# Kernel optimization log

Hardware: AMD Instinct MI355X
Metric: run time of the kernel (lower is better)

## Reference

```python
import jax, jax.numpy as jnp
import numpy as np

TAU = 1.0
NUM_CLASSES = 14
EDGE_W = 500.0
BODY_W = 200.0
LOSS_W = 1.0


def _cross_reduce(x, op, pad_val):
    """Apply op over the 3D 6-neighborhood cross (scipy default structure).
    x: bool [B, C, D, H, W]."""
    p = jnp.pad(x, ((0, 0), (0, 0), (1, 1), (1, 1), (1, 1)), constant_values=pad_val)
    r = p[:, :, 1:-1, 1:-1, 1:-1]
    r = op(r, p[:, :, :-2, 1:-1, 1:-1]); r = op(r, p[:, :, 2:, 1:-1, 1:-1])
    r = op(r, p[:, :, 1:-1, :-2, 1:-1]); r = op(r, p[:, :, 1:-1, 2:, 1:-1])
    r = op(r, p[:, :, 1:-1, 1:-1, :-2]); r = op(r, p[:, :, 1:-1, 1:-1, 2:])
    return r


def _edge_body_masks(gt_labels):
    # gt_labels: int [B, 1, D, H, W] -> bool masks [B, NUM_CLASSES, D, H, W]
    gt = gt_labels[:, 0]  # [B, D, H, W]
    onehot = gt[:, None] == jnp.arange(NUM_CLASSES, dtype=gt.dtype)[None, :, None, None, None]
    # binary_dilation ^ binary_erosion, both with border_value=0 (scipy default)
    dil = _cross_reduce(onehot, jnp.logical_or, False)
    ero = _cross_reduce(onehot, jnp.logical_and, False)
    edges = jnp.logical_xor(dil, ero)
    bodies = jnp.logical_and(jnp.logical_not(edges), onehot)
    # class 0 (background) masks are forced to zero in the original loop
    edges = edges.at[:, 0].set(False)
    bodies = bodies.at[:, 0].set(False)
    return edges, bodies


def _cwd(preds_S, preds_T):
    # ChannelWiseDivergence: per-(batch,channel) softmax over flattened spatial dims
    B, C = preds_S.shape[0], preds_S.shape[1]
    s = preds_S.reshape(B * C, -1) / TAU
    t = preds_T.reshape(B * C, -1) / TAU
    p_t = jax.nn.softmax(t, axis=-1)
    loss = jnp.sum(p_t * (jax.nn.log_softmax(t, axis=-1) - jax.nn.log_softmax(s, axis=-1)))
    return loss * (TAU ** 2) / (B * C)


def setup_inputs() -> dict:
    key = jax.random.key(0)
    k1, k2, k3 = jax.random.split(key, 3)
    B, C, D, H, W = 2, NUM_CLASSES, 96, 96, 96
    preds_S = jax.random.normal(k1, (B, C, D, H, W), dtype=jnp.float32)
    preds_T = jax.random.normal(k2, (B, C, D, H, W), dtype=jnp.float32)
    gt_labels = jax.random.randint(k3, (B, 1, D, H, W), 0, NUM_CLASSES, dtype=jnp.int64)
    return {"preds_S": preds_S, "preds_T": preds_T, "gt_labels": gt_labels}


def reference(preds_S, preds_T, gt_labels):
    B = preds_S.shape[0]
    edges, bodies = _edge_body_masks(gt_labels)
    me = edges.astype(preds_S.dtype)
    mb = bodies.astype(preds_S.dtype)
    loss_edges = _cwd(preds_S * me, preds_T * me) * LOSS_W * EDGE_W / B
    loss_bodies = _cwd(preds_S * mb, preds_T * mb) * LOSS_W * BODY_W / B
    return loss_edges, loss_bodies
```

## Files before the change

kernel.cpp:

```cpp
#include <hip/hip_runtime.h>
#include <math.h>

#define NCLS 14
#define DIMX 96
#define DIMXY (DIMX * DIMX)
#define NVOX (DIMX * DIMX * DIMX)
#define BATCH 2
#define ROWS (BATCH * NCLS)
#define TPB 256
#define BPR 54
#define VPT 16
#define BLK_VOX (TPB * 4 * VPT)
#define PSTRIDE 8

__global__ __launch_bounds__(256) void mask_kernel(const int* __restrict__ gt,
                                                   unsigned* __restrict__ masks) {
    int idx4 = blockIdx.x * 256 + threadIdx.x;
    if (idx4 >= BATCH * NVOX / 4) return;
    int v4 = idx4 * 4;
    int b = v4 / NVOX;
    int v = v4 - b * NVOX;
    int w = v % DIMX;
    int h = (v / DIMX) % DIMX;
    int d = v / DIMXY;
    const int* __restrict__ g = gt + (size_t)b * NVOX;

    int gc[4];
    { int4 t4 = *(const int4*)&g[v]; gc[0] = t4.x; gc[1] = t4.y; gc[2] = t4.z; gc[3] = t4.w; }
    bool hasU = h > 0, hasD = h < DIMX - 1, hasF = d > 0, hasB = d < DIMX - 1;
    bool hasL0 = w > 0;
    bool hasR3 = (w + 3) < DIMX - 1;
    int up[4], dn[4], fr[4], bk[4];
    if (hasU) { int4 t4 = *(const int4*)&g[v - DIMX];  up[0]=t4.x; up[1]=t4.y; up[2]=t4.z; up[3]=t4.w; }
    if (hasD) { int4 t4 = *(const int4*)&g[v + DIMX];  dn[0]=t4.x; dn[1]=t4.y; dn[2]=t4.z; dn[3]=t4.w; }
    if (hasF) { int4 t4 = *(const int4*)&g[v - DIMXY]; fr[0]=t4.x; fr[1]=t4.y; fr[2]=t4.z; fr[3]=t4.w; }
    if (hasB) { int4 t4 = *(const int4*)&g[v + DIMXY]; bk[0]=t4.x; bk[1]=t4.y; bk[2]=t4.z; bk[3]=t4.w; }
    int lf0 = hasL0 ? g[v - 1] : 0;
    int rt3 = hasR3 ? g[v + 4] : 0;

    unsigned res[4];
    #pragma unroll
    for (int j = 0; j < 4; ++j) {
        int c0 = gc[j];
        unsigned dil = 1u << c0;
        bool all = hasU && hasD && hasF && hasB;
        int  lf = (j == 0) ? lf0 : gc[j - 1]; bool hl = (j > 0) || hasL0;
        int  rt = (j == 3) ? rt3 : gc[j + 1]; bool hr = (j < 3) || hasR3;
        all = all && hl && hr;
        if (hl)   { dil |= 1u << lf;    all = all && (lf == c0); }
        if (hr)   { dil |= 1u << rt;    all = all && (rt == c0); }
        if (hasU) { dil |= 1u << up[j]; all = all && (up[j] == c0); }
        if (hasD) { dil |= 1u << dn[j]; all = all && (dn[j] == c0); }
        if (hasF) { dil |= 1u << fr[j]; all = all && (fr[j] == c0); }
        if (hasB) { dil |= 1u << bk[j]; all = all && (bk[j] == c0); }
        unsigned edge = dil & ~1u;
        if (all) edge &= ~(1u << c0);
        unsigned bodyc = (all && c0 != 0) ? (unsigned)c0 : 15u;
        res[j] = edge | (bodyc << 16);
    }
    *(uint4*)&masks[(size_t)v4] = make_uint4(res[0], res[1], res[2], res[3]);
}

__global__ __launch_bounds__(TPB) void cwd_kernel(const float* __restrict__ Sp,
                                                  const float* __restrict__ Tp,
                                                  const unsigned* __restrict__ masks,
                                                  float* __restrict__ partials) {
    int row = blockIdx.x / BPR;
    int blk = blockIdx.x - row * BPR;
    int b = row / NCLS;
    unsigned c = (unsigned)(row - b * NCLS);
    const float* __restrict__ s_ptr = Sp + (size_t)row * NVOX;
    const float* __restrict__ t_ptr = Tp + (size_t)row * NVOX;
    const unsigned* __restrict__ m_ptr = masks + (size_t)b * NVOX;
    int base = blk * BLK_VOX + (int)threadIdx.x * 4;

    float ez[4] = {0.f, 0.f, 0.f, 0.f};
    float es[4] = {0.f, 0.f, 0.f, 0.f};
    float eq[4] = {0.f, 0.f, 0.f, 0.f};
    float bz = 0.f, bs1 = 0.f, bzs = 0.f, bcnt = 0.f;

    #pragma unroll 4
    for (int k = 0; k < VPT; ++k) {
        int v = base + k * (TPB * 4);
        uint4  wm4 = *(const uint4*)&m_ptr[v];
        float4 t4  = *(const float4*)&t_ptr[v];
        float4 s4  = *(const float4*)&s_ptr[v];
        unsigned wms[4] = {wm4.x, wm4.y, wm4.z, wm4.w};
        float    ts[4]  = {t4.x, t4.y, t4.z, t4.w};
        float    ss[4]  = {s4.x, s4.y, s4.z, s4.w};
        #pragma unroll
        for (int j = 0; j < 4; ++j) {
            unsigned wm = wms[j];
            float me = (float)((wm >> c) & 1u);
            float tv = ts[j] * me;
            float sv = ss[j] * me;
            float et = __expf(tv);
            ez[j] += et;
            es[j] += et * (tv - sv);
            eq[j] += __expf(sv);
            if (((wm >> 16) & 0xFu) == c) {
                float bt = __expf(ts[j]);
                bz  += bt;
                bs1 += bt * (ts[j] - ss[j]);
                bzs += __expf(ss[j]);
                bcnt += 1.f;
            }
        }
    }
    float r0 = (ez[0] + ez[1]) + (ez[2] + ez[3]);
    float r1 = (es[0] + es[1]) + (es[2] + es[3]);
    float r2 = (eq[0] + eq[1]) + (eq[2] + eq[3]);
    float r3 = bz, r4 = bs1, r5 = bzs, r6 = bcnt;

    #pragma unroll
    for (int off = 32; off > 0; off >>= 1) {
        r0 += __shfl_down(r0, off);
        r1 += __shfl_down(r1, off);
        r2 += __shfl_down(r2, off);
        r3 += __shfl_down(r3, off);
        r4 += __shfl_down(r4, off);
        r5 += __shfl_down(r5, off);
        r6 += __shfl_down(r6, off);
    }
    __shared__ float red[4][PSTRIDE];
    int wid = (int)threadIdx.x >> 6;
    int lane = (int)threadIdx.x & 63;
    if (lane == 0) {
        red[wid][0] = r0; red[wid][1] = r1; red[wid][2] = r2; red[wid][3] = r3;
        red[wid][4] = r4; red[wid][5] = r5; red[wid][6] = r6;
    }
    __syncthreads();
    if (threadIdx.x < PSTRIDE) {
        int i = (int)threadIdx.x;
        float sum = (i < 7) ? (red[0][i] + red[1][i] + red[2][i] + red[3][i]) : 0.f;
        partials[(size_t)blockIdx.x * PSTRIDE + i] = sum;
    }
}

__global__ __launch_bounds__(64) void final_kernel(const float* __restrict__ partials,
                                                   float* __restrict__ out) {
    __shared__ double se[64], sb[64];
    int r = threadIdx.x;
    double le = 0.0, lb = 0.0;
    if (r < ROWS) {
        double zt = 0.0, s1 = 0.0, zs = 0.0;
        double vbz = 0.0, vbs1 = 0.0, vbzs = 0.0, vbc = 0.0;
        for (int k = 0; k < BPR; ++k) {
            const float* p = partials + (size_t)(r * BPR + k) * PSTRIDE;
            zt  += p[0]; s1  += p[1]; zs  += p[2];
            vbz += p[3]; vbs1 += p[4]; vbzs += p[5]; vbc += p[6];
        }
        le = s1 / zt - log(zt) + log(zs);
        double rem = (double)NVOX - vbc;
        double bzt = vbz + rem, bzs2 = vbzs + rem;
        lb = vbs1 / bzt - log(bzt) + log(bzs2);
    }
    se[r] = le;
    sb[r] = lb;
    __syncthreads();
    if (r == 0) {
        double a = 0.0, c = 0.0;
        for (int i = 0; i < ROWS; ++i) { a += se[i]; c += sb[i]; }
        out[0] = (float)(a * (500.0 / 56.0));
        out[1] = (float)(c * (200.0 / 56.0));
    }
}

extern "C" void kernel_launch(void* const* d_in, const int* in_sizes, int n_in,
                              void* d_out, int out_size, void* d_ws, size_t ws_size,
                              hipStream_t stream) {
    const float* Sp = (const float*)d_in[0];
    const float* Tp = (const float*)d_in[1];
    const int* gt = (const int*)d_in[2];
    float* out = (float*)d_out;

    unsigned* masks = (unsigned*)d_ws;
    float* partials = (float*)((char*)d_ws + (size_t)BATCH * NVOX * sizeof(unsigned));

    hipLaunchKernelGGL(mask_kernel, dim3(BATCH * NVOX / 4 / 256), dim3(256), 0, stream,
                       gt, masks);
    hipLaunchKernelGGL(cwd_kernel, dim3(ROWS * BPR), dim3(TPB), 0, stream,
                       Sp, Tp, masks, partials);
    hipLaunchKernelGGL(final_kernel, dim3(1), dim3(64), 0, stream, partials, out);
}
```

Measured before the change: 52.30 us.

## Process all classes per voxel chunk and accumulate sparse body terms atomically

Each block of the CWD kernel now covers one voxel chunk for all 14 classes of a batch, instead of one class row. The packed mask word is then loaded once per voxel rather than once per class, which removes most of the repeated mask traffic. Body-loss terms are gathered only for the voxel's body class and added to per-row accumulators with global atomics. This relies on body voxels being rare, and adds register pressure from 42 per-thread accumulators plus a wider final reduction.

```diff
diff --git a/kernel.cpp b/kernel.cpp
--- a/kernel.cpp
+++ b/kernel.cpp
@@ -8,13 +8,14 @@
 #define BATCH 2
 #define ROWS (BATCH * NCLS)
 #define TPB 256
-#define BPR 54
-#define VPT 16
-#define BLK_VOX (TPB * 4 * VPT)
-#define PSTRIDE 8
+#define VPT 2
+#define CPB (TPB * 4 * VPT)
+#define NBLK (NVOX / CPB)
 
 __global__ __launch_bounds__(256) void mask_kernel(const int* __restrict__ gt,
-                                                   unsigned* __restrict__ masks) {
+                                                   unsigned* __restrict__ masks,
+                                                   float* __restrict__ body_acc) {
+    if (blockIdx.x == 0 && threadIdx.x < ROWS * 4) body_acc[threadIdx.x] = 0.f;
     int idx4 = blockIdx.x * 256 + threadIdx.x;
     if (idx4 >= BATCH * NVOX / 4) return;
     int v4 = idx4 * 4;
@@ -64,105 +65,122 @@
 __global__ __launch_bounds__(TPB) void cwd_kernel(const float* __restrict__ Sp,
                                                   const float* __restrict__ Tp,
                                                   const unsigned* __restrict__ masks,
-                                                  float* __restrict__ partials) {
-    int row = blockIdx.x / BPR;
-    int blk = blockIdx.x - row * BPR;
-    int b = row / NCLS;
-    unsigned c = (unsigned)(row - b * NCLS);
-    const float* __restrict__ s_ptr = Sp + (size_t)row * NVOX;
-    const float* __restrict__ t_ptr = Tp + (size_t)row * NVOX;
-    const unsigned* __restrict__ m_ptr = masks + (size_t)b * NVOX;
-    int base = blk * BLK_VOX + (int)threadIdx.x * 4;
-
-    float ez[4] = {0.f, 0.f, 0.f, 0.f};
-    float es[4] = {0.f, 0.f, 0.f, 0.f};
-    float eq[4] = {0.f, 0.f, 0.f, 0.f};
-    float bz = 0.f, bs1 = 0.f, bzs = 0.f, bcnt = 0.f;
-
-    #pragma unroll 4
+                                                  float* __restrict__ partials,
+                                                  float* __restrict__ body_acc) {
+    int blk = blockIdx.x;
+    int b = blk / NBLK;
+    int chunk = blk - b * NBLK;
+    const unsigned* __restrict__ mp = masks + (size_t)b * NVOX;
+    const float* __restrict__ tb = Tp + (size_t)b * NCLS * NVOX;
+    const float* __restrict__ sb = Sp + (size_t)b * NCLS * NVOX;
+    int base = chunk * CPB + (int)threadIdx.x * 4;
+
+    float zt[NCLS], s1[NCLS], zs[NCLS];
+    #pragma unroll
+    for (int c = 0; c < NCLS; ++c) { zt[c] = 0.f; s1[c] = 0.f; zs[c] = 0.f; }
+
+    #pragma unroll
     for (int k = 0; k < VPT; ++k) {
         int v = base + k * (TPB * 4);
-        uint4  wm4 = *(const uint4*)&m_ptr[v];
-        float4 t4  = *(const float4*)&t_ptr[v];
-        float4 s4  = *(const float4*)&s_ptr[v];
-        unsigned wms[4] = {wm4.x, wm4.y, wm4.z, wm4.w};
-        float    ts[4]  = {t4.x, t4.y, t4.z, t4.w};
-        float    ss[4]  = {s4.x, s4.y, s4.z, s4.w};
+        uint4 wm4 = *(const uint4*)&mp[v];
+        unsigned wm[4] = {wm4.x, wm4.y, wm4.z, wm4.w};
+        #pragma unroll
+        for (int c = 0; c < NCLS; ++c) {
+            float4 t4 = *(const float4*)&tb[(size_t)c * NVOX + v];
+            float4 s4 = *(const float4*)&sb[(size_t)c * NVOX + v];
+            float tt[4] = {t4.x, t4.y, t4.z, t4.w};
+            float ss[4] = {s4.x, s4.y, s4.z, s4.w};
+            #pragma unroll
+            for (int j = 0; j < 4; ++j) {
+                float me = (float)((wm[j] >> c) & 1u);
+                float tv = tt[j] * me;
+                float sv = ss[j] * me;
+                float et = __expf(tv);
+                zt[c] += et;
+                s1[c] += et * (tv - sv);
+                zs[c] += __expf(sv);
+            }
+        }
         #pragma unroll
         for (int j = 0; j < 4; ++j) {
-            unsigned wm = wms[j];
-            float me = (float)((wm >> c) & 1u);
-            float tv = ts[j] * me;
-            float sv = ss[j] * me;
-            float et = __expf(tv);
-            ez[j] += et;
-            es[j] += et * (tv - sv);
-            eq[j] += __expf(sv);
-            if (((wm >> 16) & 0xFu) == c) {
-                float bt = __expf(ts[j]);
-                bz  += bt;
-                bs1 += bt * (ts[j] - ss[j]);
-                bzs += __expf(ss[j]);
-                bcnt += 1.f;
+            unsigned bc = wm[j] >> 16;
+            if (bc != 15u) {
+                size_t off = (size_t)bc * NVOX + (size_t)(v + j);
+                float t = tb[off], s = sb[off];
+                float* acc = body_acc + ((size_t)b * NCLS + bc) * 4;
+                atomicAdd(acc + 0, __expf(t));
+                atomicAdd(acc + 1, __expf(t) * (t - s));
+                atomicAdd(acc + 2, __expf(s));
+                atomicAdd(acc + 3, 1.f);
             }
         }
     }
-    float r0 = (ez[0] + ez[1]) + (ez[2] + ez[3]);
-    float r1 = (es[0] + es[1]) + (es[2] + es[3]);
-    float r2 = (eq[0] + eq[1]) + (eq[2] + eq[3]);
-    float r3 = bz, r4 = bs1, r5 = bzs, r6 = bcnt;
 
     #pragma unroll
     for (int off = 32; off > 0; off >>= 1) {
-        r0 += __shfl_down(r0, off);
-        r1 += __shfl_down(r1, off);
-        r2 += __shfl_down(r2, off);
-        r3 += __shfl_down(r3, off);
-        r4 += __shfl_down(r4, off);
-        r5 += __shfl_down(r5, off);
-        r6 += __shfl_down(r6, off);
-    }
-    __shared__ float red[4][PSTRIDE];
+        #pragma unroll
+        for (int c = 0; c < NCLS; ++c) {
+            zt[c] += __shfl_down(zt[c], off);
+            s1[c] += __shfl_down(s1[c], off);
+            zs[c] += __shfl_down(zs[c], off);
+        }
+    }
+    __shared__ float red[4][NCLS * 3];
     int wid = (int)threadIdx.x >> 6;
     int lane = (int)threadIdx.x & 63;
     if (lane == 0) {
-        red[wid][0] = r0; red[wid][1] = r1; red[wid][2] = r2; red[wid][3] = r3;
-        red[wid][4] = r4; red[wid][5] = r5; red[wid][6] = r6;
+        #pragma unroll
+        for (int c = 0; c < NCLS; ++c) {
+            red[wid][c * 3 + 0] = zt[c];
+            red[wid][c * 3 + 1] = s1[c];
+            red[wid][c * 3 + 2] = zs[c];
+        }
     }
     __syncthreads();
-    if (threadIdx.x < PSTRIDE) {
+    if (threadIdx.x < NCLS * 3) {
         int i = (int)threadIdx.x;
-        float sum = (i < 7) ? (red[0][i] + red[1][i] + red[2][i] + red[3][i]) : 0.f;
-        partials[(size_t)blockIdx.x * PSTRIDE + i] = sum;
-    }
-}
-
-__global__ __launch_bounds__(64) void final_kernel(const float* __restrict__ partials,
-                                                   float* __restrict__ out) {
-    __shared__ double se[64], sb[64];
-    int r = threadIdx.x;
-    double le = 0.0, lb = 0.0;
-    if (r < ROWS) {
+        float s = (red[0][i] + red[1][i]) + (red[2][i] + red[3][i]);
+        partials[(size_t)blk * (NCLS * 3) + i] = s;
+    }
+}
+
+__global__ __launch_bounds__(1024) void final_kernel(const float* __restrict__ partials,
+                                                     const float* __restrict__ body_acc,
+                                                     float* __restrict__ out) {
+    int tid = (int)threadIdx.x;
+    int row = tid >> 5;
+    int sub = tid & 31;
+    __shared__ double les[ROWS], lbs[ROWS];
+    if (row < ROWS) {
+        int b = row / NCLS, c = row - b * NCLS;
         double zt = 0.0, s1 = 0.0, zs = 0.0;
-        double vbz = 0.0, vbs1 = 0.0, vbzs = 0.0, vbc = 0.0;
-        for (int k = 0; k < BPR; ++k) {
-            const float* p = partials + (size_t)(r * BPR + k) * PSTRIDE;
-            zt  += p[0]; s1  += p[1]; zs  += p[2];
-            vbz += p[3]; vbs1 += p[4]; vbzs += p[5]; vbc += p[6];
-        }
-        le = s1 / zt - log(zt) + log(zs);
-        double rem = (double)NVOX - vbc;
-        double bzt = vbz + rem, bzs2 = vbzs + rem;
-        lb = vbs1 / bzt - log(bzt) + log(bzs2);
-    }
-    se[r] = le;
-    sb[r] = lb;
+        for (int k = sub; k < NBLK; k += 32) {
+            const float* p = partials + (size_t)(b * NBLK + k) * (NCLS * 3) + c * 3;
+            zt += (double)p[0]; s1 += (double)p[1]; zs += (double)p[2];
+        }
+        #pragma unroll
+        for (int off = 16; off > 0; off >>= 1) {
+            zt += __shfl_down(zt, off, 32);
+            s1 += __shfl_down(s1, off, 32);
+            zs += __shfl_down(zs, off, 32);
+        }
+        if (sub == 0) {
+            double le = s1 / zt - log(zt) + log(zs);
+            const float* a = body_acc + (size_t)row * 4;
+            double rem = (double)NVOX - (double)a[3];
+            double bzt = (double)a[0] + rem;
+            double bzs = (double)a[2] + rem;
+            double lb = (double)a[1] / bzt - log(bzt) + log(bzs);
+            les[row] = le;
+            lbs[row] = lb;
+        }
+    }
     __syncthreads();
-    if (r == 0) {
-        double a = 0.0, c = 0.0;
-        for (int i = 0; i < ROWS; ++i) { a += se[i]; c += sb[i]; }
-        out[0] = (float)(a * (500.0 / 56.0));
-        out[1] = (float)(c * (200.0 / 56.0));
+    if (tid == 0) {
+        double A = 0.0, C = 0.0;
+        for (int i = 0; i < ROWS; ++i) { A += les[i]; C += lbs[i]; }
+        out[0] = (float)(A * (500.0 / 56.0));
+        out[1] = (float)(C * (200.0 / 56.0));
     }
 }
 
@@ -176,10 +194,12 @@
 
     unsigned* masks = (unsigned*)d_ws;
     float* partials = (float*)((char*)d_ws + (size_t)BATCH * NVOX * sizeof(unsigned));
+    float* body_acc = partials + (size_t)BATCH * NBLK * (NCLS * 3);
 
     hipLaunchKernelGGL(mask_kernel, dim3(BATCH * NVOX / 4 / 256), dim3(256), 0, stream,
-                       gt, masks);
-    hipLaunchKernelGGL(cwd_kernel, dim3(ROWS * BPR), dim3(TPB), 0, stream,
-                       Sp, Tp, masks, partials);
-    hipLaunchKernelGGL(final_kernel, dim3(1), dim3(64), 0, stream, partials, out);
-}
+                       gt, masks, body_acc);
+    hipLaunchKernelGGL(cwd_kernel, dim3(BATCH * NBLK), dim3(TPB), 0, stream,
+                       Sp, Tp, masks, partials, body_acc);
+    hipLaunchKernelGGL(final_kernel, dim3(1), dim3(1024), 0, stream,
+                       partials, body_acc, out);
+}
```

After: 57.40 us. 1.1x slower.
